# Optimization experiments

Hardware: AMD Instinct MI355X
Metric: run time of the kernel (lower is better)

The kernel has to match this reference:

```python
import jax, jax.numpy as jnp
import numpy as np

N = 50000      # nodes
E = 800000     # directed edges
P = 200000     # edge pairs to score
IN_DIM = 32
HID = 64       # per-head hidden dim
HEADS = 4
D = HID * HEADS  # 256, concat output dim
NEG_SLOPE = 0.2  # PyG GATConv leaky_relu slope


def setup_inputs() -> dict:
    key = jax.random.key(0)
    ks = jax.random.split(key, 12)
    return {
        "x": jax.random.normal(ks[0], (N, IN_DIM), jnp.float32),
        "edge_index": jax.random.randint(ks[1], (2, E), 0, N),
        "edge_pairs": jax.random.randint(ks[2], (P, 2), 0, N),
        "W1": jax.random.normal(ks[3], (IN_DIM, D), jnp.float32) / np.float32(np.sqrt(IN_DIM)),
        "att_src1": jax.random.normal(ks[4], (HEADS, HID), jnp.float32) * 0.1,
        "att_dst1": jax.random.normal(ks[5], (HEADS, HID), jnp.float32) * 0.1,
        "b1": jnp.zeros((D,), jnp.float32),
        "W2": jax.random.normal(ks[6], (D, D), jnp.float32) / np.float32(np.sqrt(D)),
        "att_src2": jax.random.normal(ks[7], (HEADS, HID), jnp.float32) * 0.1,
        "att_dst2": jax.random.normal(ks[8], (HEADS, HID), jnp.float32) * 0.1,
        "b2": jnp.zeros((D,), jnp.float32),
        "head_w": jax.random.normal(ks[9], (2 * D, 1), jnp.float32) / np.float32(np.sqrt(2 * D)),
        "head_b": jnp.zeros((1,), jnp.float32),
    }


def _gat_layer(x, src, dst, W, a_src, a_dst, b):
    """PyG-style GATConv (concat=True, self-loops already appended to src/dst)."""
    n = x.shape[0]
    h = (x @ W).reshape(n, HEADS, HID)            # [N,H,C]
    alpha_s = (h * a_src).sum(-1)                  # [N,H]
    alpha_d = (h * a_dst).sum(-1)                  # [N,H]
    e = jax.nn.leaky_relu(alpha_s[src] + alpha_d[dst], NEG_SLOPE)  # [E',H]
    # segment softmax over edges grouped by destination node
    m = jax.ops.segment_max(e, dst, num_segments=n)                # [N,H]
    ex = jnp.exp(e - m[dst])
    denom = jax.ops.segment_sum(ex, dst, num_segments=n)           # [N,H]
    alpha = ex / (denom[dst] + 1e-16)                              # [E',H]
    msg = h[src] * alpha[..., None]                                # [E',H,C]
    out = jax.ops.segment_sum(msg, dst, num_segments=n)            # [N,H,C]
    return out.reshape(n, D) + b


def reference(x, edge_index, edge_pairs, W1, att_src1, att_dst1, b1,
              W2, att_src2, att_dst2, b2, head_w, head_b):
    n = x.shape[0]
    loops = jnp.arange(n, dtype=edge_index.dtype)  # add_self_loops (PyG default)
    src = jnp.concatenate([edge_index[0], loops])
    dst = jnp.concatenate([edge_index[1], loops])
    h = jax.nn.relu(_gat_layer(x, src, dst, W1, att_src1, att_dst1, b1))
    h = jax.nn.relu(_gat_layer(h, src, dst, W2, att_src2, att_dst2, b2))
    pair = jnp.concatenate([h[edge_pairs[:, 0]], h[edge_pairs[:, 1]]], axis=1)  # [P,2D]
    return (pair @ head_w + head_b).squeeze(-1)  # [P]
```

## Files before the change

### kernel.cpp

```cpp
#include <hip/hip_runtime.h>

#define N_NODES 50000
#define E_EDGES 800000
#define E_TOT   (E_EDGES + N_NODES)
#define P_PAIRS 200000
#define IN_DIM  32
#define HID     64
#define HEADS   4
#define D       256
#define NEG_SLOPE 0.2f
#define SCAN_BS 1024
#define LOG2E 1.4426950408889634f

typedef float    f32x4 __attribute__((ext_vector_type(4)));
typedef _Float16 h16x8 __attribute__((ext_vector_type(8)));
typedef _Float16 h16x4 __attribute__((ext_vector_type(4)));

__device__ __forceinline__ float ex2(float v) { return __builtin_amdgcn_exp2f(v); }

__device__ __forceinline__ void edge_sd(const int* __restrict__ ei, int e, int& s, int& d) {
  if (e < E_EDGES) { s = ei[e]; d = ei[E_EDGES + e]; }
  else             { s = d = e - E_EDGES; }
}

__global__ void count_prep_k(const int* __restrict__ ei, int* __restrict__ deg,
                             int* __restrict__ rank,
                             const float* __restrict__ W1,
                             const float* __restrict__ as1,
                             const float* __restrict__ ad1,
                             const float* __restrict__ W2,
                             float* __restrict__ wa_s, float* __restrict__ wa_d,
                             _Float16* __restrict__ Wt) {
  if (blockIdx.x < 256) {
    int g = blockIdx.x * 256 + threadIdx.x;
    int col = g >> 8, k = g & 255;
    Wt[g] = (_Float16)W2[(size_t)k * D + col];
    if (blockIdx.x == 0) {
      int t = threadIdx.x;
      int kk = (t >> 2) & 31, h = t & 3;
      const float* att = (t < 128) ? as1 : ad1;
      float sum = 0.f;
      for (int c = 0; c < HID; ++c) sum += W1[kk * D + h * HID + c] * att[h * HID + c];
      float* dst = (t < 128) ? wa_s : wa_d;
      dst[kk * 4 + h] = sum * LOG2E;
    }
  } else {
    int e = (blockIdx.x - 256) * 256 + threadIdx.x;
    if (e >= E_TOT) return;
    int s, d; edge_sd(ei, e, s, d);
    rank[e] = atomicAdd(&deg[d], 1);
  }
}

__global__ __launch_bounds__(SCAN_BS) void scan_block_k(const int* __restrict__ in,
                                                        int* __restrict__ out,
                                                        int* __restrict__ bsum, int n) {
  __shared__ int tmp[SCAN_BS];
  int g = blockIdx.x * SCAN_BS + threadIdx.x;
  tmp[threadIdx.x] = (g < n) ? in[g] : 0;
  __syncthreads();
  for (int off = 1; off < SCAN_BS; off <<= 1) {
    int t = 0;
    if ((int)threadIdx.x >= off) t = tmp[threadIdx.x - off];
    __syncthreads();
    if ((int)threadIdx.x >= off) tmp[threadIdx.x] += t;
    __syncthreads();
  }
  if (g < n) out[g] = tmp[threadIdx.x];
  if (threadIdx.x == SCAN_BS - 1) bsum[blockIdx.x] = tmp[SCAN_BS - 1];
}

__global__ void add_off_k(const int* __restrict__ scan_out,
                          const int* __restrict__ bsum,
                          int* __restrict__ rowptr) {
  int g = blockIdx.x * 256 + threadIdx.x;
  if (g >= N_NODES) return;
  int blk = g / SCAN_BS;
  int add = 0;
  for (int b = 0; b < blk; ++b) add += bsum[b];
  rowptr[g + 1] = scan_out[g] + add;
  if (g == 0) rowptr[0] = 0;
}

__global__ __launch_bounds__(256) void scatter_alphas_k(
    const int* __restrict__ ei, const int* __restrict__ rowptr,
    const int* __restrict__ rank, int* __restrict__ csr,
    const float* __restrict__ x,
    const float* __restrict__ wa_s, const float* __restrict__ wa_d,
    float* __restrict__ alps, float* __restrict__ alpd, int a1Blk) {
  if ((int)blockIdx.x < a1Blk) {
    int w = (blockIdx.x * 256 + threadIdx.x) >> 6;
    int lane = threadIdx.x & 63;
    int n = w * 8 + (lane >> 3);
    int j = lane & 7;
    float4 xv = make_float4(0.f, 0.f, 0.f, 0.f);
    if (n < N_NODES) xv = *(const float4*)(x + (size_t)n * IN_DIM + j * 4);
    float ps[4] = {0.f, 0.f, 0.f, 0.f}, pd[4] = {0.f, 0.f, 0.f, 0.f};
    #pragma unroll
    for (int kk = 0; kk < 4; ++kk) {
      float xk = ((const float*)&xv)[kk];
      float4 ws = *(const float4*)(wa_s + (j * 4 + kk) * 4);
      float4 wd = *(const float4*)(wa_d + (j * 4 + kk) * 4);
      ps[0] += xk * ws.x; ps[1] += xk * ws.y; ps[2] += xk * ws.z; ps[3] += xk * ws.w;
      pd[0] += xk * wd.x; pd[1] += xk * wd.y; pd[2] += xk * wd.z; pd[3] += xk * wd.w;
    }
    #pragma unroll
    for (int off = 1; off < 8; off <<= 1) {
      #pragma unroll
      for (int h = 0; h < 4; ++h) {
        ps[h] += __shfl_xor(ps[h], off);
        pd[h] += __shfl_xor(pd[h], off);
      }
    }
    if (j == 0 && n < N_NODES) {
      *(float4*)(alps + n * 4) = make_float4(ps[0], ps[1], ps[2], ps[3]);
      *(float4*)(alpd + n * 4) = make_float4(pd[0], pd[1], pd[2], pd[3]);
    }
  } else {
    int e = (blockIdx.x - a1Blk) * 256 + threadIdx.x;
    if (e >= E_TOT) return;
    int s, d; edge_sd(ei, e, s, d);
    csr[rowptr[d] + rank[e]] = s;
  }
}

__global__ __launch_bounds__(256) void gat_gather1_k(
    const int* __restrict__ rowptr, const int* __restrict__ csr,
    const float* __restrict__ alps, const float* __restrict__ alpd,
    const float* __restrict__ x, float* __restrict__ agg) {
  int wid2 = (blockIdx.x * 256 + threadIdx.x) >> 6;
  int lane = threadIdx.x & 63;
  int half = lane >> 5, l = lane & 31;
  int n = wid2 * 2 + half;
  bool valid = n < N_NODES;
  int q = l >> 3;
  int kk = (l & 7) * 4;
  int beg = valid ? rowptr[n] : 0;
  int end = valid ? rowptr[n + 1] : 0;
  float ad = valid ? alpd[n * HEADS + q] : 0.f;

  float den = 0.f;
  float4 acc = make_float4(0.f, 0.f, 0.f, 0.f);

  for (int i = beg; i < end; i += 8) {
    int s[8]; bool ok[8]; float xl[8]; float4 xv[8];
    #pragma unroll
    for (int j = 0; j < 8; ++j) { ok[j] = (i + j) < end; s[j] = ok[j] ? csr[i + j] : 0; }
    #pragma unroll
    for (int j = 0; j < 8; ++j) xl[j] = alps[s[j] * HEADS + q];
    #pragma unroll
    for (int j = 0; j < 8; ++j) xv[j] = *(const float4*)(x + (size_t)s[j] * IN_DIM + kk);
    float e[8];
    #pragma unroll
    for (int j = 0; j < 8; ++j) {
      float t = xl[j] + ad;
      t = fmaxf(t, NEG_SLOPE * t);
      e[j] = ok[j] ? ex2(t) : 0.f;
    }
    den += (((e[0] + e[1]) + (e[2] + e[3])) + ((e[4] + e[5]) + (e[6] + e[7])));
    #pragma unroll
    for (int j = 0; j < 8; ++j) {
      acc.x = fmaf(e[j], xv[j].x, acc.x);
      acc.y = fmaf(e[j], xv[j].y, acc.y);
      acc.z = fmaf(e[j], xv[j].z, acc.z);
      acc.w = fmaf(e[j], xv[j].w, acc.w);
    }
  }
  if (valid) {
    float inv = 1.f / (den + 1e-16f);
    float4 o = make_float4(acc.x * inv, acc.y * inv, acc.z * inv, acc.w * inv);
    *(float4*)(agg + (size_t)n * 128 + l * 4) = o;
  }
}

__global__ __launch_bounds__(256) void gemm_head1(const float* __restrict__ agg,
                                                  const float* __restrict__ W,
                                                  const float* __restrict__ b,
                                                  _Float16* __restrict__ A16) {
  __shared__ float As[32][68];
  __shared__ float Bs[32][64];
  const int row0 = blockIdx.x * 64;
  const int q = blockIdx.y;
  const int col0 = q * 64;
  const int t = threadIdx.x, tx = t & 15, ty = t >> 4;
  #pragma unroll
  for (int i = 0; i < 2; ++i) {
    int idx = t + i * 256;
    int r = idx >> 3, k4 = idx & 7;
    int rr = row0 + r;
    float4 a = make_float4(0.f, 0.f, 0.f, 0.f);
    if (rr < N_NODES) a = *(const float4*)(agg + (size_t)rr * 128 + q * 32 + k4 * 4);
    As[k4 * 4 + 0][r] = a.x;
    As[k4 * 4 + 1][r] = a.y;
    As[k4 * 4 + 2][r] = a.z;
    As[k4 * 4 + 3][r] = a.w;
  }
  #pragma unroll
  for (int i = 0; i < 2; ++i) {
    int idx = t + i * 256;
    int k = idx >> 4, c4 = idx & 15;
    *(float4*)&Bs[k][c4 * 4] = *(const float4*)(W + (size_t)k * D + col0 + c4 * 4);
  }
  __syncthreads();
  float acc[4][4] = {{0.f}};
  #pragma unroll
  for (int k = 0; k < 32; ++k) {
    float4 av = *(const float4*)&As[k][ty * 4];
    float4 bv = *(const float4*)&Bs[k][tx * 4];
    acc[0][0] += av.x * bv.x; acc[0][1] += av.x * bv.y;
    acc[0][2] += av.x * bv.z; acc[0][3] += av.x * bv.w;
    acc[1][0] += av.y * bv.x; acc[1][1] += av.y * bv.y;
    acc[1][2] += av.y * bv.z; acc[1][3] += av.y * bv.w;
    acc[2][0] += av.z * bv.x; acc[2][1] += av.z * bv.y;
    acc[2][2] += av.z * bv.z; acc[2][3] += av.z * bv.w;
    acc[3][0] += av.w * bv.x; acc[3][1] += av.w * bv.y;
    acc[3][2] += av.w * bv.z; acc[3][3] += av.w * bv.w;
  }
  float4 bv = *(const float4*)(b + col0 + tx * 4);
  const float bb[4] = {bv.x, bv.y, bv.z, bv.w};
  #pragma unroll
  for (int i = 0; i < 4; ++i) {
    int rr = row0 + ty * 4 + i;
    if (rr < N_NODES) {
      h16x4 o4;
      #pragma unroll
      for (int j = 0; j < 4; ++j)
        o4[j] = (_Float16)fmaxf(acc[i][j] + bb[j], 0.f);
      *(h16x4*)(A16 + (size_t)rr * D + col0 + tx * 4) = o4;
    }
  }
}

__global__ __launch_bounds__(256) void gemm2_mfma(
    const _Float16* __restrict__ A16, const _Float16* __restrict__ Wt,
    const float* __restrict__ asrc, const float* __restrict__ adst,
    _Float16* __restrict__ h2, float* __restrict__ alps, float* __restrict__ alpd) {
  __shared__ __attribute__((aligned(16))) _Float16 As[128][40];
  __shared__ __attribute__((aligned(16))) _Float16 Bs[128][40];
  const int row0 = blockIdx.x * 128;
  const int col0 = blockIdx.y * 128;
  const int t = threadIdx.x;
  const int wave = t >> 6, lane = t & 63;
  const int wr = wave >> 1, wc = wave & 1;
  const int lg = lane >> 4, li = lane & 15;

  f32x4 acc[4][4];
  #pragma unroll
  for (int m = 0; m < 4; ++m)
    #pragma unroll
    for (int n = 0; n < 4; ++n) acc[m][n] = (f32x4)0.f;

  for (int kc = 0; kc < D; kc += 32) {
    #pragma unroll
    for (int i = 0; i < 2; ++i) {
      int idx = t + i * 256;
      int r = idx >> 2, seg = idx & 3;
      int rr = row0 + r;
      uint4 va = make_uint4(0, 0, 0, 0);
      if (rr < N_NODES) va = *(const uint4*)(A16 + (size_t)rr * D + kc + seg * 8);
      *(uint4*)&As[r][seg * 8] = va;
      uint4 vb = *(const uint4*)(Wt + (size_t)(col0 + r) * D + kc + seg * 8);
      *(uint4*)&Bs[r][seg * 8] = vb;
    }
    __syncthreads();
    h16x8 af[4], bf[4];
    #pragma unroll
    for (int m = 0; m < 4; ++m)
      af[m] = *(const h16x8*)&As[wr * 64 + m * 16 + li][lg * 8];
    #pragma unroll
    for (int n = 0; n < 4; ++n)
      bf[n] = *(const h16x8*)&Bs[wc * 64 + n * 16 + li][lg * 8];
    #pragma unroll
    for (int m = 0; m < 4; ++m)
      #pragma unroll
      for (int n = 0; n < 4; ++n)
        acc[m][n] = __builtin_amdgcn_mfma_f32_16x16x32_f16(af[m], bf[n], acc[m][n], 0, 0, 0);
    __syncthreads();
  }

  #pragma unroll
  for (int m = 0; m < 4; ++m) {
    #pragma unroll
    for (int reg = 0; reg < 4; ++reg) {
      int rr = row0 + wr * 64 + m * 16 + lg * 4 + reg;
      if (rr < N_NODES) {
        #pragma unroll
        for (int n = 0; n < 4; ++n)
          h2[(size_t)rr * D + col0 + wc * 64 + n * 16 + li] = (_Float16)acc[m][n][reg];
      }
    }
  }

  const int q = blockIdx.y * 2 + wc;
  float wsv[4], wdv[4];
  #pragma unroll
  for (int n = 0; n < 4; ++n) {
    wsv[n] = asrc[q * HID + n * 16 + li];
    wdv[n] = adst[q * HID + n * 16 + li];
  }
  #pragma unroll
  for (int m = 0; m < 4; ++m) {
    #pragma unroll
    for (int reg = 0; reg < 4; ++reg) {
      float ps = acc[m][0][reg] * wsv[0] + acc[m][1][reg] * wsv[1]
               + acc[m][2][reg] * wsv[2] + acc[m][3][reg] * wsv[3];
      float pd = acc[m][0][reg] * wdv[0] + acc[m][1][reg] * wdv[1]
               + acc[m][2][reg] * wdv[2] + acc[m][3][reg] * wdv[3];
      #pragma unroll
      for (int off = 1; off < 16; off <<= 1) {
        ps += __shfl_xor(ps, off);
        pd += __shfl_xor(pd, off);
      }
      int rr = row0 + wr * 64 + m * 16 + lg * 4 + reg;
      if (li == 0 && rr < N_NODES) {
        alps[rr * HEADS + q] = ps * LOG2E;
        alpd[rr * HEADS + q] = pd * LOG2E;
      }
    }
  }
}

__global__ __launch_bounds__(256) void gat_gather2_k(
    const int* __restrict__ rowptr, const int* __restrict__ csr,
    const float* __restrict__ alps, const float* __restrict__ alpd,
    const _Float16* __restrict__ h, const float* __restrict__ b,
    const float* __restrict__ hw,
    float* __restrict__ u, float* __restrict__ v) {
  int wid2 = (blockIdx.x * 256 + threadIdx.x) >> 6;
  int lane = threadIdx.x & 63;
  int half = lane >> 5, l = lane & 31;
  int n = wid2 * 2 + half;
  bool valid = n < N_NODES;
  int q = l >> 3;
  int beg = valid ? rowptr[n] : 0;
  int end = valid ? rowptr[n + 1] : 0;
  float ad = valid ? alpd[n * HEADS + q] : 0.f;

  float den = 0.f;
  float acc[8] = {0.f, 0.f, 0.f, 0.f, 0.f, 0.f, 0.f, 0.f};

  for (int i = beg; i < end; i += 6) {
    int s[6]; bool ok[6]; float xl[6]; h16x8 hv[6];
    #pragma unroll
    for (int j = 0; j < 6; ++j) { ok[j] = (i + j) < end; s[j] = ok[j] ? csr[i + j] : 0; }
    #pragma unroll
    for (int j = 0; j < 6; ++j) xl[j] = alps[s[j] * HEADS + q];
    #pragma unroll
    for (int j = 0; j < 6; ++j) hv[j] = *(const h16x8*)(h + (size_t)s[j] * D + l * 8);
    float e[6];
    #pragma unroll
    for (int j = 0; j < 6; ++j) {
      float t = xl[j] + ad;
      t = fmaxf(t, NEG_SLOPE * t);
      e[j] = ok[j] ? ex2(t) : 0.f;
    }
    den += ((e[0] + e[1]) + (e[2] + e[3])) + (e[4] + e[5]);
    #pragma unroll
    for (int ch = 0; ch < 8; ++ch) {
      float a = acc[ch];
      a = fmaf((float)hv[0][ch], e[0], a);
      a = fmaf((float)hv[1][ch], e[1], a);
      a = fmaf((float)hv[2][ch], e[2], a);
      a = fmaf((float)hv[3][ch], e[3], a);
      a = fmaf((float)hv[4][ch], e[4], a);
      a = fmaf((float)hv[5][ch], e[5], a);
      acc[ch] = a;
    }
  }

  float inv = 1.f / (den + 1e-16f);
  float4 b0 = *(const float4*)(b + l * 8);
  float4 b1 = *(const float4*)(b + l * 8 + 4);
  float4 w00 = *(const float4*)(hw + l * 8);
  float4 w01 = *(const float4*)(hw + l * 8 + 4);
  float4 w10 = *(const float4*)(hw + D + l * 8);
  float4 w11 = *(const float4*)(hw + D + l * 8 + 4);
  const float* bb[2] = {(const float*)&b0, (const float*)&b1};
  const float* w0p[2] = {(const float*)&w00, (const float*)&w01};
  const float* w1p[2] = {(const float*)&w10, (const float*)&w11};
  float su = 0.f, sv = 0.f;
  #pragma unroll
  for (int ch = 0; ch < 8; ++ch) {
    float o = fmaxf(acc[ch] * inv + bb[ch >> 2][ch & 3], 0.f);
    su = fmaf(o, w0p[ch >> 2][ch & 3], su);
    sv = fmaf(o, w1p[ch >> 2][ch & 3], sv);
  }
  #pragma unroll
  for (int off = 16; off; off >>= 1) {
    su += __shfl_xor(su, off);
    sv += __shfl_xor(sv, off);
  }
  if (l == 0 && valid) { u[n] = su; v[n] = sv; }
}

__global__ void pair_lu_k(const int* __restrict__ pairs,
                          const float* __restrict__ u, const float* __restrict__ v,
                          const float* __restrict__ hb, float* __restrict__ out) {
  int g = blockIdx.x * 256 + threadIdx.x;
  if (g >= P_PAIRS) return;
  int a = pairs[g * 2], b = pairs[g * 2 + 1];
  out[g] = u[a] + v[b] + hb[0];
}

extern "C" void kernel_launch(void* const* d_in, const int* in_sizes, int n_in,
                              void* d_out, int out_size, void* d_ws, size_t ws_size,
                              hipStream_t stream) {
  const float* x    = (const float*)d_in[0];
  const int*   ei   = (const int*)d_in[1];
  const int*   prs  = (const int*)d_in[2];
  const float* W1   = (const float*)d_in[3];
  const float* as1  = (const float*)d_in[4];
  const float* ad1  = (const float*)d_in[5];
  const float* b1   = (const float*)d_in[6];
  const float* W2   = (const float*)d_in[7];
  const float* as2  = (const float*)d_in[8];
  const float* ad2  = (const float*)d_in[9];
  const float* b2   = (const float*)d_in[10];
  const float* hw   = (const float*)d_in[11];
  const float* hb   = (const float*)d_in[12];
  float* out = (float*)d_out;

  const int NPAD = 50048;

  char* w = (char*)d_ws;
  float* buf0 = (float*)w;             w += (size_t)N_NODES * D * 4;
  float* alps = (float*)w;             w += (size_t)N_NODES * HEADS * 4;
  float* alpd = (float*)w;             w += (size_t)N_NODES * HEADS * 4;
  int* rowptr = (int*)w;               w += (size_t)(N_NODES + 1) * 4;
  int* csr    = (int*)w;               w += (size_t)E_TOT * 4;
  float* uu   = (float*)w;             w += (size_t)N_NODES * 4;
  float* vv   = (float*)w;             w += (size_t)N_NODES * 4;
  float* wa_s = (float*)w;             w += 128 * 4;
  float* wa_d = (float*)w;             w += 128 * 4;
  _Float16* A16 = (_Float16*)w;        w += (size_t)NPAD * D * 2;
  _Float16* Wt  = (_Float16*)w;        w += (size_t)D * D * 2;

  _Float16* h2f16 = (_Float16*)buf0;

  int* deg      = (int*)buf0;
  int* scan_out = deg + N_NODES;
  int* bsum     = scan_out + N_NODES;
  int* rank     = bsum + 64;

  const int eBlk     = (E_TOT + 255) / 256;
  const int nScanBlk = (N_NODES + SCAN_BS - 1) / SCAN_BS;
  const int nBlk256  = (N_NODES + 255) / 256;
  const int a1Blk    = (N_NODES * 8 + 255) / 256;
  const int g1Blk    = ((N_NODES + 1) / 2 * 64 + 255) / 256;
  const int pairBlk  = (P_PAIRS + 255) / 256;
  const dim3 headGrid((N_NODES + 63) / 64, HEADS);
  const dim3 mfmaGrid(NPAD / 128, D / 128);

  hipMemsetAsync(deg, 0, (size_t)N_NODES * 4, stream);
  count_prep_k<<<256 + eBlk, 256, 0, stream>>>(ei, deg, rank,
                                               W1, as1, ad1, W2, wa_s, wa_d, Wt);
  scan_block_k<<<nScanBlk, SCAN_BS, 0, stream>>>(deg, scan_out, bsum, N_NODES);
  add_off_k<<<nBlk256, 256, 0, stream>>>(scan_out, bsum, rowptr);
  scatter_alphas_k<<<a1Blk + eBlk, 256, 0, stream>>>(ei, rowptr, rank, csr,
                                                     x, wa_s, wa_d, alps, alpd, a1Blk);

  gat_gather1_k<<<g1Blk, 256, 0, stream>>>(rowptr, csr, alps, alpd, x, buf0);
  gemm_head1<<<headGrid, 256, 0, stream>>>(buf0, W1, b1, A16);

  gemm2_mfma<<<mfmaGrid, 256, 0, stream>>>(A16, Wt, as2, ad2, h2f16, alps, alpd);
  gat_gather2_k<<<g1Blk, 256, 0, stream>>>(rowptr, csr, alps, alpd, h2f16, b2, hw, uu, vv);

  pair_lu_k<<<pairBlk, 256, 0, stream>>>(prs, uu, vv, hb, out);
}
```

Measured before the change: 311.2 us.

## Use fp16 MFMA for layer-1 per-head projection and store aggregation in fp16

The layer-1 aggregation output is now written in fp16 instead of fp32, which halves that intermediate's traffic. The fp32 LDS-tiled per-head GEMM is replaced with a small MFMA 16x16x32 kernel. A transposed fp16 copy of W1 is built in the prep kernel for it. This cuts memory traffic and ALU work in the layer-1 GEMM, at the cost of fp16 rounding of the aggregated features and W1.

```diff
diff --git a/kernel.cpp b/kernel.cpp
--- a/kernel.cpp
+++ b/kernel.cpp
@@ -30,7 +30,7 @@
                              const float* __restrict__ ad1,
                              const float* __restrict__ W2,
                              float* __restrict__ wa_s, float* __restrict__ wa_d,
-                             _Float16* __restrict__ Wt) {
+                             _Float16* __restrict__ Wt, _Float16* __restrict__ Wt1) {
   if (blockIdx.x < 256) {
     int g = blockIdx.x * 256 + threadIdx.x;
     int col = g >> 8, k = g & 255;
@@ -44,8 +44,12 @@
       float* dst = (t < 128) ? wa_s : wa_d;
       dst[kk * 4 + h] = sum * LOG2E;
     }
+  } else if (blockIdx.x < 288) {
+    int g = (blockIdx.x - 256) * 256 + threadIdx.x;
+    int col = g >> 5, k = g & 31;
+    Wt1[g] = (_Float16)W1[(size_t)k * D + col];
   } else {
-    int e = (blockIdx.x - 256) * 256 + threadIdx.x;
+    int e = (blockIdx.x - 288) * 256 + threadIdx.x;
     if (e >= E_TOT) return;
     int s, d; edge_sd(ei, e, s, d);
     rank[e] = atomicAdd(&deg[d], 1);
@@ -127,7 +131,7 @@
 __global__ __launch_bounds__(256) void gat_gather1_k(
     const int* __restrict__ rowptr, const int* __restrict__ csr,
     const float* __restrict__ alps, const float* __restrict__ alpd,
-    const float* __restrict__ x, float* __restrict__ agg) {
+    const float* __restrict__ x, _Float16* __restrict__ agg16) {
   int wid2 = (blockIdx.x * 256 + threadIdx.x) >> 6;
   int lane = threadIdx.x & 63;
   int half = lane >> 5, l = lane & 31;
@@ -168,65 +172,48 @@
   }
   if (valid) {
     float inv = 1.f / (den + 1e-16f);
-    float4 o = make_float4(acc.x * inv, acc.y * inv, acc.z * inv, acc.w * inv);
-    *(float4*)(agg + (size_t)n * 128 + l * 4) = o;
-  }
-}
-
-__global__ __launch_bounds__(256) void gemm_head1(const float* __restrict__ agg,
-                                                  const float* __restrict__ W,
-                                                  const float* __restrict__ b,
-                                                  _Float16* __restrict__ A16) {
-  __shared__ float As[32][68];
-  __shared__ float Bs[32][64];
-  const int row0 = blockIdx.x * 64;
+    h16x4 o;
+    o[0] = (_Float16)(acc.x * inv);
+    o[1] = (_Float16)(acc.y * inv);
+    o[2] = (_Float16)(acc.z * inv);
+    o[3] = (_Float16)(acc.w * inv);
+    *(h16x4*)(agg16 + (size_t)n * 128 + l * 4) = o;
+  }
+}
+
+__global__ __launch_bounds__(256) void gemm_head1_mfma(
+    const _Float16* __restrict__ agg16, const _Float16* __restrict__ Wt1,
+    const float* __restrict__ b, _Float16* __restrict__ A16) {
+  const int t = threadIdx.x;
+  const int wave = t >> 6, lane = t & 63;
+  const int lg = lane >> 4, li = lane & 15;
   const int q = blockIdx.y;
-  const int col0 = q * 64;
-  const int t = threadIdx.x, tx = t & 15, ty = t >> 4;
-  #pragma unroll
-  for (int i = 0; i < 2; ++i) {
-    int idx = t + i * 256;
-    int r = idx >> 3, k4 = idx & 7;
-    int rr = row0 + r;
-    float4 a = make_float4(0.f, 0.f, 0.f, 0.f);
-    if (rr < N_NODES) a = *(const float4*)(agg + (size_t)rr * 128 + q * 32 + k4 * 4);
-    As[k4 * 4 + 0][r] = a.x;
-    As[k4 * 4 + 1][r] = a.y;
-    As[k4 * 4 + 2][r] = a.z;
-    As[k4 * 4 + 3][r] = a.w;
-  }
-  #pragma unroll
-  for (int i = 0; i < 2; ++i) {
-    int idx = t + i * 256;
-    int k = idx >> 4, c4 = idx & 15;
-    *(float4*)&Bs[k][c4 * 4] = *(const float4*)(W + (size_t)k * D + col0 + c4 * 4);
-  }
-  __syncthreads();
-  float acc[4][4] = {{0.f}};
-  #pragma unroll
-  for (int k = 0; k < 32; ++k) {
-    float4 av = *(const float4*)&As[k][ty * 4];
-    float4 bv = *(const float4*)&Bs[k][tx * 4];
-    acc[0][0] += av.x * bv.x; acc[0][1] += av.x * bv.y;
-    acc[0][2] += av.x * bv.z; acc[0][3] += av.x * bv.w;
-    acc[1][0] += av.y * bv.x; acc[1][1] += av.y * bv.y;
-    acc[1][2] += av.y * bv.z; acc[1][3] += av.y * bv.w;
-    acc[2][0] += av.z * bv.x; acc[2][1] += av.z * bv.y;
-    acc[2][2] += av.z * bv.z; acc[2][3] += av.z * bv.w;
-    acc[3][0] += av.w * bv.x; acc[3][1] += av.w * bv.y;
-    acc[3][2] += av.w * bv.z; acc[3][3] += av.w * bv.w;
-  }
-  float4 bv = *(const float4*)(b + col0 + tx * 4);
-  const float bb[4] = {bv.x, bv.y, bv.z, bv.w};
-  #pragma unroll
-  for (int i = 0; i < 4; ++i) {
-    int rr = row0 + ty * 4 + i;
-    if (rr < N_NODES) {
-      h16x4 o4;
-      #pragma unroll
-      for (int j = 0; j < 4; ++j)
-        o4[j] = (_Float16)fmaxf(acc[i][j] + bb[j], 0.f);
-      *(h16x4*)(A16 + (size_t)rr * D + col0 + tx * 4) = o4;
+  const int row0 = blockIdx.x * 64 + wave * 16;
+
+  h16x8 af = {};
+  int arow = row0 + li;
+  if (arow < N_NODES)
+    af = *(const h16x8*)(agg16 + (size_t)arow * 128 + q * 32 + lg * 8);
+
+  h16x8 bf[4];
+  #pragma unroll
+  for (int n = 0; n < 4; ++n)
+    bf[n] = *(const h16x8*)(Wt1 + (size_t)(q * 64 + n * 16 + li) * 32 + lg * 8);
+
+  f32x4 acc[4];
+  #pragma unroll
+  for (int n = 0; n < 4; ++n)
+    acc[n] = __builtin_amdgcn_mfma_f32_16x16x32_f16(af, bf[n], (f32x4)0.f, 0, 0, 0);
+
+  #pragma unroll
+  for (int n = 0; n < 4; ++n) {
+    int col = q * 64 + n * 16 + li;
+    float bb = b[col];
+    #pragma unroll
+    for (int reg = 0; reg < 4; ++reg) {
+      int rr = row0 + lg * 4 + reg;
+      if (rr < N_NODES)
+        A16[(size_t)rr * D + col] = (_Float16)fmaxf(acc[n][reg] + bb, 0.f);
     }
   }
 }
@@ -434,7 +421,9 @@
   float* wa_d = (float*)w;             w += 128 * 4;
   _Float16* A16 = (_Float16*)w;        w += (size_t)NPAD * D * 2;
   _Float16* Wt  = (_Float16*)w;        w += (size_t)D * D * 2;
-
+  _Float16* Wt1 = (_Float16*)w;        w += (size_t)D * IN_DIM * 2;
+
+  _Float16* agg16 = (_Float16*)buf0;
   _Float16* h2f16 = (_Float16*)buf0;
 
   int* deg      = (int*)buf0;
@@ -452,15 +441,15 @@
   const dim3 mfmaGrid(NPAD / 128, D / 128);
 
   hipMemsetAsync(deg, 0, (size_t)N_NODES * 4, stream);
-  count_prep_k<<<256 + eBlk, 256, 0, stream>>>(ei, deg, rank,
-                                               W1, as1, ad1, W2, wa_s, wa_d, Wt);
+  count_prep_k<<<288 + eBlk, 256, 0, stream>>>(ei, deg, rank,
+                                               W1, as1, ad1, W2, wa_s, wa_d, Wt, Wt1);
   scan_block_k<<<nScanBlk, SCAN_BS, 0, stream>>>(deg, scan_out, bsum, N_NODES);
   add_off_k<<<nBlk256, 256, 0, stream>>>(scan_out, bsum, rowptr);
   scatter_alphas_k<<<a1Blk + eBlk, 256, 0, stream>>>(ei, rowptr, rank, csr,
                                                      x, wa_s, wa_d, alps, alpd, a1Blk);
 
-  gat_gather1_k<<<g1Blk, 256, 0, stream>>>(rowptr, csr, alps, alpd, x, buf0);
-  gemm_head1<<<headGrid, 256, 0, stream>>>(buf0, W1, b1, A16);
+  gat_gather1_k<<<g1Blk, 256, 0, stream>>>(rowptr, csr, alps, alpd, x, agg16);
+  gemm_head1_mfma<<<headGrid, 256, 0, stream>>>(agg16, Wt1, b1, A16);
 
   gemm2_mfma<<<mfmaGrid, 256, 0, stream>>>(A16, Wt, as2, ad2, h2f16, alps, alpd);
   gat_gather2_k<<<g1Blk, 256, 0, stream>>>(rowptr, csr, alps, alpd, h2f16, b2, hw, uu, vv);
```

Result: faster. 286.7 us (-7.9%).
